# Performance work log

Hardware: AMD Instinct MI355X
Metric: run time of the kernel (lower is better)

Reference implementation:

```python
import jax, jax.numpy as jnp
import numpy as np
import math

H, W, STEPS, DT = 224, 224, 10, 0.15
B = 256

def _neighbor_sum(x):
    # 4-neighbor sum via zero-padded shifts == conv2d with the cross kernel, padding=1
    p = jnp.pad(x, ((0, 0), (0, 0), (1, 1), (1, 1)))
    return (p[:, :, :-2, 1:-1] + p[:, :, 2:, 1:-1]
            + p[:, :, 1:-1, :-2] + p[:, :, 1:-1, 2:])

def setup_inputs() -> dict:
    key = jax.random.key(0)
    k1, _ = jax.random.split(key)
    x_img = jax.random.uniform(k1, (B, 1, H, W), dtype=jnp.float32)  # in [0,1]
    omega = jnp.zeros((1, 1, H, W), dtype=jnp.float32)
    K = jnp.asarray(0.5, dtype=jnp.float32)
    return {"x_img": x_img, "omega": omega, "K": K}

def reference(x_img, omega, K):
    theta = math.pi * (2.0 * x_img - 1.0)  # (B,1,H,W)
    for _ in range(STEPS):
        sin_t = jnp.sin(theta)
        cos_t = jnp.cos(theta)
        sin_n = _neighbor_sum(sin_t)
        cos_n = _neighbor_sum(cos_t)
        # sum_neighbors sin(theta_n - theta) = cos_t*sin_n - sin_t*cos_n
        coupling = cos_t * sin_n - sin_t * cos_n
        theta = theta + DT * (omega + K * coupling)
    feat = jnp.concatenate([jnp.cos(theta), jnp.sin(theta)], axis=1)  # (B,2,H,W)
    return feat.reshape(feat.shape[0], -1)  # (B, 2*H*W)
```

## Files before the change

### kernel.cpp

```cpp
#include <hip/hip_runtime.h>

#define HH 224
#define WW 224
#define HWSZ (HH * WW)
#define NSTEPS 10
#define TH 32
#define CR 52
#define NSTRIPS 7
#define DT_C 0.15f
#define EXHALF (2 * 5 * CR)

typedef __fp16 h2 __attribute__((ext_vector_type(2)));

__device__ __forceinline__ int pack_sc(float s, float c) {
    h2 v = __builtin_amdgcn_cvt_pkrtz(s, c);
    union { h2 h; int i; } u; u.h = v;
    return u.i;
}
__device__ __forceinline__ void unpack_sc(int b, float& s, float& c) {
    union { int i; h2 h; } u; u.i = b;
    s = (float)u.h.x; c = (float)u.h.y;
}

__global__ __launch_bounds__(256)
void kuramoto_fused(const float* __restrict__ x_img,
                    const float* __restrict__ omega,
                    const float* __restrict__ Kp,
                    float* __restrict__ out)
{
    const int tx    = threadIdx.x;
    const int wv    = tx >> 6;
    const int lane  = tx & 63;
    const int strip = blockIdx.x;
    const int img   = blockIdx.y;
    const int y0    = strip * TH - NSTEPS;

    __shared__ int exf[2 * EXHALF];
    for (int i = tx; i < 2 * EXHALF; i += 256) exf[i] = 0;

    const float DTK = DT_C * Kp[0];

    float s[CR], c[CR], dtom[CR];
    const bool xin = (tx < WW);
    const float* xrow = x_img + (size_t)img * HWSZ;

    #pragma unroll
    for (int y = 0; y < CR; ++y) {
        const int gy  = y0 + y;
        const bool in = xin && (gy >= 0) && (gy < HH);
        float xv = 0.f, om = 0.f;
        if (in) {
            xv = xrow[gy * WW + tx];
            om = omega[gy * WW + tx];
        }
        const float th = fmaf(6.28318530718f, xv, -3.14159265359f);
        s[y]    = in ? __sinf(th) : 0.f;
        c[y]    = in ? __cosf(th) : 0.f;
        dtom[y] = DT_C * om;
    }

    const bool bnd  = (lane == 0) || (lane == 63);
    const int  rIdx = (lane == 63) ? ((1 * 5 + (wv + 1)) * CR) : ((0 * 5 + wv) * CR);
    const int  wIdx = (lane == 63) ? ((0 * 5 + (wv + 1)) * CR) : ((1 * 5 + wv) * CR);

    __syncthreads();
    if (bnd) {
        #pragma unroll
        for (int y = 1; y <= CR - 2; ++y)
            exf[wIdx + y] = pack_sc(s[y], c[y]);
    }
    __syncthreads();

    #pragma unroll 1
    for (int t = 0; t < NSTEPS; ++t) {
        const int cur = (t & 1) ? EXHALF : 0;
        const int nxt = EXHALF - cur;
        float sm = s[0], cm = c[0];
        float s0 = s[1], c0 = c[1];
        #pragma unroll
        for (int y = 1; y <= CR - 2; ++y) {
            const float sp = s[y + 1], cp = c[y + 1];
            const int pk = pack_sc(s0, c0);
            int up = __shfl_up(pk, 1);
            int dn = __shfl_down(pk, 1);
            const int bv = exf[cur + rIdx + y];
            if (lane == 0)  up = bv;
            if (lane == 63) dn = bv;
            float sl, cl, sr, cr2;
            unpack_sc(up, sl, cl);
            unpack_sc(dn, sr, cr2);
            const float sn   = (sm + sp) + (sl + sr);
            const float cn   = (cm + cp) + (cl + cr2);
            const float coup = fmaf(c0, sn, -(s0 * cn));
            const float d    = fmaf(DTK, coup, dtom[y]);
            const float d2   = d * d;
            const float sd   = d * fmaf(d2, fmaf(d2, 8.33333333e-3f, -1.66666667e-1f), 1.f);
            const float cd   = fmaf(d2, fmaf(d2, 4.16666667e-2f, -5.0e-1f), 1.f);
            const float ns   = fmaf(c0, sd, s0 * cd);
            const float nc   = fmaf(-s0, sd, c0 * cd);
            s[y] = ns; c[y] = nc;
            if (bnd) exf[nxt + wIdx + y] = pack_sc(ns, nc);
            sm = s0; cm = c0; s0 = sp; c0 = cp;
        }
        __syncthreads();
    }

    if (xin) {
        float* ob = out + (size_t)img * (2 * HWSZ);
        #pragma unroll
        for (int y = NSTEPS; y < NSTEPS + TH; ++y) {
            const int gy = y0 + y;
            ob[gy * WW + tx]          = c[y];
            ob[HWSZ + gy * WW + tx]   = s[y];
        }
    }
}

extern "C" void kernel_launch(void* const* d_in, const int* in_sizes, int n_in,
                              void* d_out, int out_size, void* d_ws, size_t ws_size,
                              hipStream_t stream)
{
    const float* x_img = (const float*)d_in[0];
    const float* omega = (const float*)d_in[1];
    const float* K     = (const float*)d_in[2];
    float* out = (float*)d_out;
    const int B = in_sizes[0] / HWSZ;
    dim3 grid(NSTRIPS, B);
    kuramoto_fused<<<grid, dim3(256), 0, stream>>>(x_img, omega, K, out);
}
```

Before: 429.3 us.

## Store per-thread sin/cos column state as packed fp16 to cut registers

```diff
diff --git a/kernel.cpp b/kernel.cpp
--- a/kernel.cpp
+++ b/kernel.cpp
@@ -17,12 +17,14 @@
     union { h2 h; int i; } u; u.h = v;
     return u.i;
 }
-__device__ __forceinline__ void unpack_sc(int b, float& s, float& c) {
-    union { int i; h2 h; } u; u.i = b;
-    s = (float)u.h.x; c = (float)u.h.y;
+__device__ __forceinline__ float unpk0(int b) {
+    union { int i; h2 h; } u; u.i = b; return (float)u.h[0];
+}
+__device__ __forceinline__ float unpk1(int b) {
+    union { int i; h2 h; } u; u.i = b; return (float)u.h[1];
 }
 
-__global__ __launch_bounds__(256)
+__global__ __launch_bounds__(256, 4)
 void kuramoto_fused(const float* __restrict__ x_img,
                     const float* __restrict__ omega,
                     const float* __restrict__ Kp,
@@ -40,23 +42,30 @@
 
     const float DTK = DT_C * Kp[0];
 
-    float s[CR], c[CR], dtom[CR];
+    int st[CR];
+    int dt2[CR / 2];
     const bool xin = (tx < WW);
     const float* xrow = x_img + (size_t)img * HWSZ;
 
     #pragma unroll
-    for (int y = 0; y < CR; ++y) {
-        const int gy  = y0 + y;
-        const bool in = xin && (gy >= 0) && (gy < HH);
-        float xv = 0.f, om = 0.f;
-        if (in) {
-            xv = xrow[gy * WW + tx];
-            om = omega[gy * WW + tx];
+    for (int y = 0; y < CR; y += 2) {
+        float d01[2];
+        #pragma unroll
+        for (int k = 0; k < 2; ++k) {
+            const int gy  = y0 + y + k;
+            const bool in = xin && (gy >= 0) && (gy < HH);
+            float xv = 0.f, om = 0.f;
+            if (in) {
+                xv = xrow[gy * WW + tx];
+                om = omega[gy * WW + tx];
+            }
+            const float th = fmaf(6.28318530718f, xv, -3.14159265359f);
+            const float sv = in ? __sinf(th) : 0.f;
+            const float cv = in ? __cosf(th) : 0.f;
+            st[y + k] = pack_sc(sv, cv);
+            d01[k] = DT_C * om;
         }
-        const float th = fmaf(6.28318530718f, xv, -3.14159265359f);
-        s[y]    = in ? __sinf(th) : 0.f;
-        c[y]    = in ? __cosf(th) : 0.f;
-        dtom[y] = DT_C * om;
+        dt2[y >> 1] = pack_sc(d01[0], d01[1]);
     }
 
     const bool bnd  = (lane == 0) || (lane == 63);
@@ -67,7 +76,7 @@
     if (bnd) {
         #pragma unroll
         for (int y = 1; y <= CR - 2; ++y)
-            exf[wIdx + y] = pack_sc(s[y], c[y]);
+            exf[wIdx + y] = st[y];
     }
     __syncthreads();
 
@@ -75,32 +84,34 @@
     for (int t = 0; t < NSTEPS; ++t) {
         const int cur = (t & 1) ? EXHALF : 0;
         const int nxt = EXHALF - cur;
-        float sm = s[0], cm = c[0];
-        float s0 = s[1], c0 = c[1];
+        float sm = unpk0(st[0]), cm = unpk1(st[0]);
+        float s0 = unpk0(st[1]), c0 = unpk1(st[1]);
+        int   pk0 = st[1];
         #pragma unroll
         for (int y = 1; y <= CR - 2; ++y) {
-            const float sp = s[y + 1], cp = c[y + 1];
-            const int pk = pack_sc(s0, c0);
-            int up = __shfl_up(pk, 1);
-            int dn = __shfl_down(pk, 1);
+            const int   pkp = st[y + 1];
+            const float sp = unpk0(pkp), cp = unpk1(pkp);
+            int up = __shfl_up(pk0, 1);
+            int dn = __shfl_down(pk0, 1);
             const int bv = exf[cur + rIdx + y];
             if (lane == 0)  up = bv;
             if (lane == 63) dn = bv;
-            float sl, cl, sr, cr2;
-            unpack_sc(up, sl, cl);
-            unpack_sc(dn, sr, cr2);
+            const float sl = unpk0(up), cl = unpk1(up);
+            const float sr = unpk0(dn), cr2 = unpk1(dn);
             const float sn   = (sm + sp) + (sl + sr);
             const float cn   = (cm + cp) + (cl + cr2);
             const float coup = fmaf(c0, sn, -(s0 * cn));
-            const float d    = fmaf(DTK, coup, dtom[y]);
+            const float dty  = (y & 1) ? unpk1(dt2[y >> 1]) : unpk0(dt2[y >> 1]);
+            const float d    = fmaf(DTK, coup, dty);
             const float d2   = d * d;
             const float sd   = d * fmaf(d2, fmaf(d2, 8.33333333e-3f, -1.66666667e-1f), 1.f);
             const float cd   = fmaf(d2, fmaf(d2, 4.16666667e-2f, -5.0e-1f), 1.f);
             const float ns   = fmaf(c0, sd, s0 * cd);
             const float nc   = fmaf(-s0, sd, c0 * cd);
-            s[y] = ns; c[y] = nc;
-            if (bnd) exf[nxt + wIdx + y] = pack_sc(ns, nc);
-            sm = s0; cm = c0; s0 = sp; c0 = cp;
+            const int npk = pack_sc(ns, nc);
+            st[y] = npk;
+            if (bnd) exf[nxt + wIdx + y] = npk;
+            sm = s0; cm = c0; s0 = sp; c0 = cp; pk0 = pkp;
         }
         __syncthreads();
     }
@@ -110,8 +121,8 @@
         #pragma unroll
         for (int y = NSTEPS; y < NSTEPS + TH; ++y) {
             const int gy = y0 + y;
-            ob[gy * WW + tx]          = c[y];
-            ob[HWSZ + gy * WW + tx]   = s[y];
+            ob[gy * WW + tx]          = unpk1(st[y]);
+            ob[HWSZ + gy * WW + tx]   = unpk0(st[y]);
         }
     }
 }
```

Result: faster. 351.8 us (-18.0%).
